# Optimization experiments

Hardware: AMD Instinct MI355X
Metric: run time of the kernel (lower is better)

The kernel has to match this reference:

```python
import jax, jax.numpy as jnp
import numpy as np

B, N, C = 2, 2048, 768
H = 16
D = C // H  # head_dim = 48
SCALE = 1.0 / float(np.sqrt(D))


def setup_inputs() -> dict:
    key = jax.random.key(0)
    ks = jax.random.split(key, 5)
    x = jax.random.normal(ks[0], (B, N, C), dtype=jnp.float32)
    # torch nn.Linear weights are [out, in]; apply as x @ W.T
    qkv_w = jax.random.normal(ks[1], (3 * C, C), dtype=jnp.float32) * 0.02
    qkv_b = jax.random.normal(ks[2], (3 * C,), dtype=jnp.float32) * 0.02
    proj_w = jax.random.normal(ks[3], (C, C), dtype=jnp.float32) * 0.02
    proj_b = jax.random.normal(ks[4], (C,), dtype=jnp.float32) * 0.02
    return {"x": x, "qkv_w": qkv_w, "qkv_b": qkv_b, "proj_w": proj_w, "proj_b": proj_b}


def reference(x, qkv_w, qkv_b, proj_w, proj_b):
    # qkv: (B, N, 3C) -> (3, B, H, N, D)
    qkv = x @ qkv_w.T + qkv_b
    qkv = qkv.reshape(B, N, 3, H, D).transpose(2, 0, 3, 1, 4)
    q, k, v = qkv[0], qkv[1], qkv[2]
    # manual attention: full (B, H, N, N) score matrix, as in the original
    attn = jnp.einsum('bhqd,bhkd->bhqk', q, k) * SCALE
    attn = jax.nn.softmax(attn, axis=-1)
    # attn_drop with p=0.0 (eval / deterministic) is identity
    y = jnp.einsum('bhqk,bhkd->bhqd', attn, v)
    y = y.transpose(0, 2, 1, 3).reshape(B, N, C)
    return y @ proj_w.T + proj_b
```

## Files before the change

### kernel.cpp

```cpp
#include <hip/hip_runtime.h>

typedef short v8s __attribute__((ext_vector_type(8)));
typedef short v4s __attribute__((ext_vector_type(4)));
typedef float v4f __attribute__((ext_vector_type(4)));
typedef unsigned uint2v __attribute__((ext_vector_type(2)));
typedef unsigned uint4v __attribute__((ext_vector_type(4)));
typedef unsigned short u16;

#define NSEQ 2048
#define CDIM 768
#define NH   16
#define DH   48
#define DP   64
#define MROWS 4096
#define N3C  2304
#define BH   32

#if __has_builtin(__builtin_amdgcn_exp2f)
#define EXP2(x) __builtin_amdgcn_exp2f(x)
#else
#define EXP2(x) exp2f(x)
#endif
#if __has_builtin(__builtin_amdgcn_rcpf)
#define RCP(x) __builtin_amdgcn_rcpf(x)
#else
#define RCP(x) (1.0f/(x))
#endif

#if __has_builtin(__builtin_amdgcn_permlane32_swap) && __has_builtin(__builtin_amdgcn_permlane16_swap)
#define HAVE_PERMSWAP 1
#endif

__device__ __forceinline__ u16 f2bf(float f){
  unsigned u = __float_as_uint(f);
  u += 0x7FFFu + ((u>>16)&1u);
  return (u16)(u>>16);
}

#if __has_builtin(__builtin_amdgcn_cvt_pk_bf16_f32)
typedef __bf16 bf16x2_t __attribute__((ext_vector_type(2)));
__device__ __forceinline__ unsigned pkbf(float a, float b){
  bf16x2_t r = __builtin_amdgcn_cvt_pk_bf16_f32(a, b);
  return __builtin_bit_cast(unsigned, r);
}
#else
__device__ __forceinline__ unsigned pkbf(float a, float b){
  unsigned x = __float_as_uint(a), y = __float_as_uint(b);
  x += 0x7FFFu + ((x>>16)&1u);
  y += 0x7FFFu + ((y>>16)&1u);
  return (x>>16) | (y & 0xFFFF0000u);
}
#endif

__device__ __forceinline__ void load_lds16(const u16* g, u16* l){
  __builtin_amdgcn_global_load_lds((const __attribute__((address_space(1))) void*)g,
                                   (__attribute__((address_space(3))) void*)l, 16, 0, 0);
}

#define XN8  (MROWS*CDIM/8)
#define WN8  (N3C*CDIM/8)
#define PN8  (CDIM*CDIM/8)
#define CONVB ((XN8+WN8+PN8)/256)
__global__ __launch_bounds__(256) void prep(const float* __restrict__ x, const float* __restrict__ w,
                                            const float* __restrict__ pw, u16* __restrict__ dst,
                                            u16* __restrict__ q, u16* __restrict__ k){
  int bid = blockIdx.x;
  if (bid < CONVB){
    int i = bid*256 + threadIdx.x;
    const float* src;
    if (i < XN8)            src = x  + (size_t)i*8;
    else if (i < XN8+WN8)   src = w  + (size_t)(i - XN8)*8;
    else                    src = pw + (size_t)(i - XN8 - WN8)*8;
    v4f f0 = ((const v4f*)src)[0];
    v4f f1 = ((const v4f*)src)[1];
    v8s o;
#pragma unroll
    for (int j = 0; j < 4; j++) ((u16*)&o)[j]   = f2bf(f0[j]);
#pragma unroll
    for (int j = 0; j < 4; j++) ((u16*)&o)[4+j] = f2bf(f1[j]);
    ((v8s*)dst)[i] = o;
  } else {
    int idx = (bid - CONVB)*256 + threadIdx.x;
    v8s z = (v8s){0,0,0,0,0,0,0,0};
    int r = idx >> 1, half = idx & 1;
    *(v8s*)(q + (size_t)r*DP + DH + half*8) = z;
    *(v8s*)(k + (size_t)r*DP + DH + half*8) = z;
  }
}

__global__ __launch_bounds__(256) void qkv_gemm(const u16* __restrict__ x, const u16* __restrict__ w,
                                                const float* __restrict__ bias,
                                                u16* __restrict__ q, u16* __restrict__ k, u16* __restrict__ v){
  __shared__ __align__(16) u16 As[128*32];
  __shared__ __align__(16) u16 Bs[128*32];
  const int wave = threadIdx.x >> 6;
  const int lane = threadIdx.x & 63;
  const int l15  = lane & 15;
  const int quad = lane >> 4;
  const int wm = wave & 1, wn = wave >> 1;
  const int m0 = blockIdx.x*128, n0 = blockIdx.y*128;

  const int srow = lane >> 2;
  const int sg   = (lane & 3) ^ ((lane >> 3) & 3);
  const int sgoff = sg*8;

  v4f acc[4][4];
#pragma unroll
  for (int i = 0; i < 4; i++)
#pragma unroll
    for (int j = 0; j < 4; j++) acc[i][j] = (v4f){0.f,0.f,0.f,0.f};

  const int sig = (l15 >> 1) & 3;

  for (int kt = 0; kt < CDIM/32; kt++){
    const int k0 = kt*32;
    __syncthreads();
#pragma unroll
    for (int j = 0; j < 2; j++){
      int c = wave*2 + j;
      int r = c*16 + srow;
      load_lds16(x + (size_t)(m0 + r)*CDIM + k0 + sgoff, &As[c*512]);
      load_lds16(w + (size_t)(n0 + r)*CDIM + k0 + sgoff, &Bs[c*512]);
    }
    __syncthreads();

    v8s af[4], bf[4];
#pragma unroll
    for (int t = 0; t < 4; t++){
      int ra = wm*64 + t*16 + l15;
      af[t] = *(const v8s*)(&As[ra*32 + ((quad ^ sig)<<3)]);
      int rb = wn*64 + t*16 + l15;
      bf[t] = *(const v8s*)(&Bs[rb*32 + ((quad ^ sig)<<3)]);
    }
#pragma unroll
    for (int ti = 0; ti < 4; ti++)
#pragma unroll
      for (int tj = 0; tj < 4; tj++)
        acc[ti][tj] = __builtin_amdgcn_mfma_f32_16x16x32_bf16(af[ti], bf[tj], acc[ti][tj], 0, 0, 0);
  }

  const float QS = 0.2082540589f;
#pragma unroll
  for (int tj = 0; tj < 4; tj++){
    const int c = n0 + wn*64 + tj*16 + l15;
    const float bv = bias[c];
    const int t = c / CDIM;
    const int rem = c - t*CDIM;
    const int h = rem / DH;
    const int d = rem - h*DH;
#pragma unroll
    for (int ti = 0; ti < 4; ti++){
#pragma unroll
      for (int r = 0; r < 4; r++){
        int m = m0 + wm*64 + ti*16 + quad*4 + r;
        int b_ = m >> 11;
        int n  = m & (NSEQ-1);
        float val = acc[ti][tj][r] + bv;
        if (t == 0) val *= QS;
        u16 o  = f2bf(val);
        int bhn = b_*NH + h;
        if (t == 0)      q[((size_t)bhn*NSEQ + n)*DP + d] = o;
        else if (t == 1) k[((size_t)bhn*NSEQ + n)*DP + d] = o;
        else             v[((size_t)bhn*DP + d)*NSEQ + n] = o;
      }
    }
  }
}

__global__ __launch_bounds__(256, 4) void attn(const u16* __restrict__ q, const u16* __restrict__ k,
                                               const u16* __restrict__ v,
                                               float* __restrict__ oacc, float* __restrict__ lacc){
  __shared__ __align__(16) u16 Kl[2][64*64];
  __shared__ __align__(16) u16 Vl[2][48*64];
#ifndef HAVE_PERMSWAP
  __shared__ __align__(16) u16 Pl[4*2*1024];
#endif
  const int bh = blockIdx.x;
  const int qt = blockIdx.y;
  const int sp = blockIdx.z;
  const int wave = threadIdx.x >> 6;
  const int lane = threadIdx.x & 63;
  const int l15  = lane & 15;
  const int quad = lane >> 4;
  const int lo3  = l15 & 7;
  const u16* qb = q + (size_t)bh*NSEQ*DP;
  const u16* kb = k + (size_t)bh*NSEQ*DP;
  const u16* vb = v + (size_t)bh*DP*NSEQ;
  const int qm = qt*128 + wave*32;

  v8s qf[2][2];
#pragma unroll
  for (int si = 0; si < 2; si++)
#pragma unroll
    for (int ks = 0; ks < 2; ks++)
      qf[si][ks] = *(const v8s*)(qb + (size_t)(qm + si*16 + l15)*DP + ks*32 + quad*8);

  const short one = (short)0x3F80;
  const v8s vones = (l15 == 0) ? (v8s){one,one,one,one,one,one,one,one}
                               : (v8s){0,0,0,0,0,0,0,0};

  v4f o[2][4];
#pragma unroll
  for (int si = 0; si < 2; si++)
#pragma unroll
    for (int i = 0; i < 4; i++) o[si][i] = (v4f){0.f,0.f,0.f,0.f};

  const int sr  = lane >> 3;
  const int soff = ((lane & 7) ^ (sr & 7)) * 8;
#ifndef HAVE_PERMSWAP
  u16* Plw = Pl + wave*2048;
#endif

  const int krow0 = wave*8 + sr;
#define STAGE(kt_, b_) do{                                                              \
    load_lds16(kb + ((size_t)((kt_)*64 + krow0))*DP + soff,      &Kl[b_][krow0*64]);    \
    load_lds16(kb + ((size_t)((kt_)*64 + 32 + krow0))*DP + soff, &Kl[b_][(32+krow0)*64]);\
    load_lds16(vb + (size_t)krow0*NSEQ + (kt_)*64 + soff,        &Vl[b_][krow0*64]);    \
    if (wave < 2)                                                                       \
      load_lds16(vb + (size_t)(32+krow0)*NSEQ + (kt_)*64 + soff, &Vl[b_][(32+krow0)*64]);\
  } while(0)

  STAGE(sp*16, 0);

  for (int i = 0; i < 16; i++){
    const int buf = i & 1;
    __syncthreads();
    if (i < 15) STAGE(sp*16 + i + 1, buf^1);

    const u16* Klb = &Kl[buf][0];
    const u16* Vlb = &Vl[buf][0];

    v4f s[2][4];
#pragma unroll
    for (int nt = 0; nt < 4; nt++){
      int rrow = nt*16 + l15;
      v8s kf0 = *(const v8s*)(&Klb[rrow*64 + ((quad ^ lo3)<<3)]);
      v8s kf1 = *(const v8s*)(&Klb[rrow*64 + (((4+quad) ^ lo3)<<3)]);
      s[0][nt] = __builtin_amdgcn_mfma_f32_16x16x32_bf16(kf0, qf[0][0], (v4f){0.f,0.f,0.f,0.f}, 0, 0, 0);
      s[0][nt] = __builtin_amdgcn_mfma_f32_16x16x32_bf16(kf1, qf[0][1], s[0][nt], 0, 0, 0);
      s[1][nt] = __builtin_amdgcn_mfma_f32_16x16x32_bf16(kf0, qf[1][0], (v4f){0.f,0.f,0.f,0.f}, 0, 0, 0);
      s[1][nt] = __builtin_amdgcn_mfma_f32_16x16x32_bf16(kf1, qf[1][1], s[1][nt], 0, 0, 0);
    }

    v8s pa[2][2];
#ifdef HAVE_PERMSWAP
#pragma unroll
    for (int si = 0; si < 2; si++){
      unsigned w[4][2];
#pragma unroll
      for (int nt = 0; nt < 4; nt++){
        w[nt][0] = pkbf(EXP2(s[si][nt][0]), EXP2(s[si][nt][1]));
        w[nt][1] = pkbf(EXP2(s[si][nt][2]), EXP2(s[si][nt][3]));
      }
#pragma unroll
      for (int ks = 0; ks < 2; ks++){
        unsigned W[4];
#pragma unroll
        for (int h = 0; h < 2; h++){
          auto a = __builtin_amdgcn_permlane32_swap(w[2*ks][h], w[2*ks+1][h], false, false);
          auto b = __builtin_amdgcn_permlane16_swap(a[0], a[1], false, false);
          W[h]   = b[0];
          W[2+h] = b[1];
        }
        uint4v u; u[0] = W[0]; u[1] = W[1]; u[2] = W[2]; u[3] = W[3];
        pa[si][ks] = __builtin_bit_cast(v8s, u);
      }
    }
#else
#pragma unroll
    for (int si = 0; si < 2; si++)
#pragma unroll
      for (int nt = 0; nt < 4; nt++){
        uint2v pw;
        pw.x = pkbf(EXP2(s[si][nt][0]), EXP2(s[si][nt][1]));
        pw.y = pkbf(EXP2(s[si][nt][2]), EXP2(s[si][nt][3]));
        int g = nt*2 + (quad>>1);
        *(uint2v*)(&Plw[si*1024 + l15*64 + ((g ^ lo3)<<3) + (quad&1)*4]) = pw;
      }
#pragma unroll
    for (int si = 0; si < 2; si++)
#pragma unroll
      for (int ks = 0; ks < 2; ks++){
        int ga = ks*4 + quad;
        pa[si][ks] = *(const v8s*)(&Plw[si*1024 + l15*64 + ((ga ^ lo3)<<3)]);
      }
#endif

#pragma unroll
    for (int dt = 0; dt < 3; dt++){
#pragma unroll
      for (int ks = 0; ks < 2; ks++){
        int row = dt*16 + l15;
        v8s vf = *(const v8s*)(&Vlb[row*64 + (((ks*4+quad) ^ lo3)<<3)]);
        o[0][dt] = __builtin_amdgcn_mfma_f32_16x16x32_bf16(pa[0][ks], vf, o[0][dt], 0, 0, 0);
        o[1][dt] = __builtin_amdgcn_mfma_f32_16x16x32_bf16(pa[1][ks], vf, o[1][dt], 0, 0, 0);
      }
    }
#pragma unroll
    for (int ks = 0; ks < 2; ks++){
      o[0][3] = __builtin_amdgcn_mfma_f32_16x16x32_bf16(pa[0][ks], vones, o[0][3], 0, 0, 0);
      o[1][3] = __builtin_amdgcn_mfma_f32_16x16x32_bf16(pa[1][ks], vones, o[1][3], 0, 0, 0);
    }
  }

  const int b_ = bh / NH, h = bh % NH;
  float* oa = oacc + (size_t)sp*MROWS*CDIM;
  float* la = lacc + (size_t)sp*MROWS*NH;
#pragma unroll
  for (int si = 0; si < 2; si++){
#pragma unroll
    for (int r = 0; r < 4; r++){
      int rowg = b_*NSEQ + qm + si*16 + quad*4 + r;
#pragma unroll
      for (int dt = 0; dt < 3; dt++)
        oa[(size_t)rowg*CDIM + h*DH + dt*16 + l15] = o[si][dt][r];
      if (l15 == 0) la[rowg*NH + h] = o[si][3][r];
    }
  }
}

__global__ __launch_bounds__(256) void finalize(const float* __restrict__ oacc,
                                                const float* __restrict__ lacc,
                                                u16* __restrict__ y){
  int i = blockIdx.x*256 + threadIdx.x;
  int rowg = i / 192, c4 = i - rowg*192;
  int c = c4*4, h = c / DH;
  float l = lacc[rowg*NH + h] + lacc[MROWS*NH + rowg*NH + h];
  float inv = RCP(l);
  v4f a = *(const v4f*)(oacc + (size_t)rowg*CDIM + c);
  v4f b = *(const v4f*)(oacc + (size_t)MROWS*CDIM + (size_t)rowg*CDIM + c);
  v4s o4;
#pragma unroll
  for (int j = 0; j < 4; j++) o4[j] = (short)f2bf((a[j] + b[j])*inv);
  *(v4s*)(y + (size_t)rowg*CDIM + c) = o4;
}

__global__ __launch_bounds__(256) void proj_gemm(const u16* __restrict__ y, const u16* __restrict__ w,
                                                 const float* __restrict__ bias, float* __restrict__ out){
  __shared__ __align__(16) u16 As[64*32];
  __shared__ __align__(16) u16 Bs[128*32];
  const int wave = threadIdx.x >> 6;
  const int lane = threadIdx.x & 63;
  const int l15  = lane & 15;
  const int quad = lane >> 4;
  const int wm = wave & 1, wn = wave >> 1;
  const int m0 = blockIdx.x*64, n0 = blockIdx.y*128;

  const int srow = lane >> 2;
  const int sg   = (lane & 3) ^ ((lane >> 3) & 3);
  const int sgoff = sg*8;

  v4f acc[2][4];
#pragma unroll
  for (int i = 0; i < 2; i++)
#pragma unroll
    for (int j = 0; j < 4; j++) acc[i][j] = (v4f){0.f,0.f,0.f,0.f};

  const int sig = (l15 >> 1) & 3;

  for (int kt = 0; kt < CDIM/32; kt++){
    const int k0 = kt*32;
    __syncthreads();
    {
      int rA = wave*16 + srow;
      load_lds16(y + (size_t)(m0 + rA)*CDIM + k0 + sgoff, &As[wave*512]);
#pragma unroll
      for (int j = 0; j < 2; j++){
        int c = wave*2 + j;
        int rB = c*16 + srow;
        load_lds16(w + (size_t)(n0 + rB)*CDIM + k0 + sgoff, &Bs[c*512]);
      }
    }
    __syncthreads();

    v8s af[2], bf[4];
#pragma unroll
    for (int t = 0; t < 2; t++){
      int ra = wm*32 + t*16 + l15;
      af[t] = *(const v8s*)(&As[ra*32 + ((quad ^ sig)<<3)]);
    }
#pragma unroll
    for (int t = 0; t < 4; t++){
      int rb = wn*64 + t*16 + l15;
      bf[t] = *(const v8s*)(&Bs[rb*32 + ((quad ^ sig)<<3)]);
    }
#pragma unroll
    for (int ti = 0; ti < 2; ti++)
#pragma unroll
      for (int tj = 0; tj < 4; tj++)
        acc[ti][tj] = __builtin_amdgcn_mfma_f32_16x16x32_bf16(af[ti], bf[tj], acc[ti][tj], 0, 0, 0);
  }

#pragma unroll
  for (int tj = 0; tj < 4; tj++){
    const int c = n0 + wn*64 + tj*16 + l15;
    const float bv = bias[c];
#pragma unroll
    for (int ti = 0; ti < 2; ti++){
#pragma unroll
      for (int r = 0; r < 4; r++){
        int m = m0 + wm*32 + ti*16 + quad*4 + r;
        out[(size_t)m*CDIM + c] = acc[ti][tj][r] + bv;
      }
    }
  }
}

extern "C" void kernel_launch(void* const* d_in, const int* in_sizes, int n_in,
                              void* d_out, int out_size, void* d_ws, size_t ws_size,
                              hipStream_t stream){
  const float* x      = (const float*)d_in[0];
  const float* qkv_w  = (const float*)d_in[1];
  const float* qkv_b  = (const float*)d_in[2];
  const float* proj_w = (const float*)d_in[3];
  const float* proj_b = (const float*)d_in[4];
  float* out = (float*)d_out;

  u16* xb  = (u16*)d_ws;
  u16* wb  = xb  + (size_t)MROWS*CDIM;
  u16* pwb = wb  + (size_t)N3C*CDIM;
  u16* q   = pwb + (size_t)CDIM*CDIM;
  u16* k   = q + (size_t)BH*NSEQ*DP;
  u16* v   = k + (size_t)BH*NSEQ*DP;
  float* oacc = (float*)(v + (size_t)BH*NSEQ*DP);
  float* lacc = oacc + (size_t)2*MROWS*CDIM;
  u16* y = xb;

  prep<<<dim3(CONVB + 512), dim3(256), 0, stream>>>(x, qkv_w, proj_w, xb, q, k);
  qkv_gemm<<<dim3(MROWS/128, N3C/128), dim3(256), 0, stream>>>(xb, wb, qkv_b, q, k, v);
  attn<<<dim3(BH, NSEQ/128, 2), dim3(256), 0, stream>>>(q, k, v, oacc, lacc);
  finalize<<<dim3(MROWS*192/256), dim3(256), 0, stream>>>(oacc, lacc, y);
  proj_gemm<<<dim3(MROWS/64, CDIM/128), dim3(256), 0, stream>>>(y, pwb, proj_b, out);
}
```

Baseline: 168.1 us.

## Double-buffer LDS in QKV and projection GEMMs, shrink projection tile

Both GEMM kernels now use two LDS buffers. The next k-tile's global-to-LDS load is issued right after a single barrier, so it overlaps with the MFMA work on the current tile, and one of the two barriers per iteration is removed. The projection GEMM tile also shrinks from 64x128 to 64x64, which doubles the number of blocks for better occupancy across CUs. This relies on the barrier waiting for the outstanding async LDS loads. The change uses more LDS in the QKV GEMM and does less work per block in the projection GEMM.

```diff
diff --git a/kernel.cpp b/kernel.cpp
--- a/kernel.cpp
+++ b/kernel.cpp
@@ -91,8 +91,8 @@
 __global__ __launch_bounds__(256) void qkv_gemm(const u16* __restrict__ x, const u16* __restrict__ w,
                                                 const float* __restrict__ bias,
                                                 u16* __restrict__ q, u16* __restrict__ k, u16* __restrict__ v){
-  __shared__ __align__(16) u16 As[128*32];
-  __shared__ __align__(16) u16 Bs[128*32];
+  __shared__ __align__(16) u16 As[2][128*32];
+  __shared__ __align__(16) u16 Bs[2][128*32];
   const int wave = threadIdx.x >> 6;
   const int lane = threadIdx.x & 63;
   const int l15  = lane & 15;
@@ -112,25 +112,30 @@
 
   const int sig = (l15 >> 1) & 3;
 
+#define QSTAGE(kt_, b_) do{                                                         \
+    _Pragma("unroll")                                                               \
+    for (int j = 0; j < 2; j++){                                                    \
+      int c = wave*2 + j;                                                           \
+      int r = c*16 + srow;                                                          \
+      load_lds16(x + (size_t)(m0 + r)*CDIM + (kt_)*32 + sgoff, &As[b_][c*512]);     \
+      load_lds16(w + (size_t)(n0 + r)*CDIM + (kt_)*32 + sgoff, &Bs[b_][c*512]);     \
+    }                                                                               \
+  } while(0)
+
+  QSTAGE(0, 0);
+
   for (int kt = 0; kt < CDIM/32; kt++){
-    const int k0 = kt*32;
+    const int buf = kt & 1;
     __syncthreads();
-#pragma unroll
-    for (int j = 0; j < 2; j++){
-      int c = wave*2 + j;
-      int r = c*16 + srow;
-      load_lds16(x + (size_t)(m0 + r)*CDIM + k0 + sgoff, &As[c*512]);
-      load_lds16(w + (size_t)(n0 + r)*CDIM + k0 + sgoff, &Bs[c*512]);
-    }
-    __syncthreads();
+    if (kt < CDIM/32 - 1) QSTAGE(kt+1, buf^1);
 
     v8s af[4], bf[4];
 #pragma unroll
     for (int t = 0; t < 4; t++){
       int ra = wm*64 + t*16 + l15;
-      af[t] = *(const v8s*)(&As[ra*32 + ((quad ^ sig)<<3)]);
+      af[t] = *(const v8s*)(&As[buf][ra*32 + ((quad ^ sig)<<3)]);
       int rb = wn*64 + t*16 + l15;
-      bf[t] = *(const v8s*)(&Bs[rb*32 + ((quad ^ sig)<<3)]);
+      bf[t] = *(const v8s*)(&Bs[buf][rb*32 + ((quad ^ sig)<<3)]);
     }
 #pragma unroll
     for (int ti = 0; ti < 4; ti++)
@@ -138,6 +143,7 @@
       for (int tj = 0; tj < 4; tj++)
         acc[ti][tj] = __builtin_amdgcn_mfma_f32_16x16x32_bf16(af[ti], bf[tj], acc[ti][tj], 0, 0, 0);
   }
+#undef QSTAGE
 
   const float QS = 0.2082540589f;
 #pragma unroll
@@ -337,63 +343,59 @@
 
 __global__ __launch_bounds__(256) void proj_gemm(const u16* __restrict__ y, const u16* __restrict__ w,
                                                  const float* __restrict__ bias, float* __restrict__ out){
-  __shared__ __align__(16) u16 As[64*32];
-  __shared__ __align__(16) u16 Bs[128*32];
+  __shared__ __align__(16) u16 As[2][64*32];
+  __shared__ __align__(16) u16 Bs[2][64*32];
   const int wave = threadIdx.x >> 6;
   const int lane = threadIdx.x & 63;
   const int l15  = lane & 15;
   const int quad = lane >> 4;
   const int wm = wave & 1, wn = wave >> 1;
-  const int m0 = blockIdx.x*64, n0 = blockIdx.y*128;
+  const int m0 = blockIdx.x*64, n0 = blockIdx.y*64;
 
   const int srow = lane >> 2;
   const int sg   = (lane & 3) ^ ((lane >> 3) & 3);
   const int sgoff = sg*8;
 
-  v4f acc[2][4];
+  v4f acc[2][2];
 #pragma unroll
   for (int i = 0; i < 2; i++)
 #pragma unroll
-    for (int j = 0; j < 4; j++) acc[i][j] = (v4f){0.f,0.f,0.f,0.f};
+    for (int j = 0; j < 2; j++) acc[i][j] = (v4f){0.f,0.f,0.f,0.f};
 
   const int sig = (l15 >> 1) & 3;
+  const int rS = wave*16 + srow;
+
+#define PSTAGE(kt_, b_) do{                                                          \
+    load_lds16(y + (size_t)(m0 + rS)*CDIM + (kt_)*32 + sgoff, &As[b_][wave*512]);    \
+    load_lds16(w + (size_t)(n0 + rS)*CDIM + (kt_)*32 + sgoff, &Bs[b_][wave*512]);    \
+  } while(0)
+
+  PSTAGE(0, 0);
 
   for (int kt = 0; kt < CDIM/32; kt++){
-    const int k0 = kt*32;
+    const int buf = kt & 1;
     __syncthreads();
-    {
-      int rA = wave*16 + srow;
-      load_lds16(y + (size_t)(m0 + rA)*CDIM + k0 + sgoff, &As[wave*512]);
-#pragma unroll
-      for (int j = 0; j < 2; j++){
-        int c = wave*2 + j;
-        int rB = c*16 + srow;
-        load_lds16(w + (size_t)(n0 + rB)*CDIM + k0 + sgoff, &Bs[c*512]);
-      }
-    }
-    __syncthreads();
-
-    v8s af[2], bf[4];
+    if (kt < CDIM/32 - 1) PSTAGE(kt+1, buf^1);
+
+    v8s af[2], bf[2];
 #pragma unroll
     for (int t = 0; t < 2; t++){
       int ra = wm*32 + t*16 + l15;
-      af[t] = *(const v8s*)(&As[ra*32 + ((quad ^ sig)<<3)]);
-    }
-#pragma unroll
-    for (int t = 0; t < 4; t++){
-      int rb = wn*64 + t*16 + l15;
-      bf[t] = *(const v8s*)(&Bs[rb*32 + ((quad ^ sig)<<3)]);
+      af[t] = *(const v8s*)(&As[buf][ra*32 + ((quad ^ sig)<<3)]);
+      int rb = wn*32 + t*16 + l15;
+      bf[t] = *(const v8s*)(&Bs[buf][rb*32 + ((quad ^ sig)<<3)]);
     }
 #pragma unroll
     for (int ti = 0; ti < 2; ti++)
 #pragma unroll
-      for (int tj = 0; tj < 4; tj++)
+      for (int tj = 0; tj < 2; tj++)
         acc[ti][tj] = __builtin_amdgcn_mfma_f32_16x16x32_bf16(af[ti], bf[tj], acc[ti][tj], 0, 0, 0);
   }
-
-#pragma unroll
-  for (int tj = 0; tj < 4; tj++){
-    const int c = n0 + wn*64 + tj*16 + l15;
+#undef PSTAGE
+
+#pragma unroll
+  for (int tj = 0; tj < 2; tj++){
+    const int c = n0 + wn*32 + tj*16 + l15;
     const float bv = bias[c];
 #pragma unroll
     for (int ti = 0; ti < 2; ti++){
@@ -430,5 +432,5 @@
   qkv_gemm<<<dim3(MROWS/128, N3C/128), dim3(256), 0, stream>>>(xb, wb, qkv_b, q, k, v);
   attn<<<dim3(BH, NSEQ/128, 2), dim3(256), 0, stream>>>(q, k, v, oacc, lacc);
   finalize<<<dim3(MROWS*192/256), dim3(256), 0, stream>>>(oacc, lacc, y);
-  proj_gemm<<<dim3(MROWS/64, CDIM/128), dim3(256), 0, stream>>>(y, pwb, proj_b, out);
-}
+  proj_gemm<<<dim3(MROWS/64, CDIM/64), dim3(256), 0, stream>>>(y, pwb, proj_b, out);
+}
```

Result: slower. 177.7 us (+5.7%).

## Store Q transposed with permlane-packed vector epilogue stores and add MFMA setprio

Applied to the files above, without the earlier changes.

Q now uses a d-major layout like V, so the QKV GEMM epilogue for Q and V can pack bf16 pairs, shuffle them with permlane swaps and write 16-byte vector stores instead of scattered 2-byte stores. The attention kernel gathers Q fragments with strided scalar loads, issued after the first K/V stage so they overlap it. The zero-padding kernel is adjusted to the new Q layout. s_setprio is raised around the MFMA blocks to favour matrix issue across waves. The strided Q gather is an extra cost paid once per attention block.

```diff
diff --git a/kernel.cpp b/kernel.cpp
--- a/kernel.cpp
+++ b/kernel.cpp
@@ -83,8 +83,10 @@
     int idx = (bid - CONVB)*256 + threadIdx.x;
     v8s z = (v8s){0,0,0,0,0,0,0,0};
     int r = idx >> 1, half = idx & 1;
-    *(v8s*)(q + (size_t)r*DP + DH + half*8) = z;
     *(v8s*)(k + (size_t)r*DP + DH + half*8) = z;
+    int bhn = idx >> 12, rem = idx & 4095;
+    int dd = rem >> 8, nc = rem & 255;
+    *(v8s*)(q + ((size_t)bhn*DP + DH + dd)*NSEQ + nc*8) = z;
   }
 }
 
@@ -140,28 +142,66 @@
   }
 
   const float QS = 0.2082540589f;
-#pragma unroll
-  for (int tj = 0; tj < 4; tj++){
-    const int c = n0 + wn*64 + tj*16 + l15;
-    const float bv = bias[c];
-    const int t = c / CDIM;
-    const int rem = c - t*CDIM;
-    const int h = rem / DH;
-    const int d = rem - h*DH;
-#pragma unroll
-    for (int ti = 0; ti < 4; ti++){
-#pragma unroll
-      for (int r = 0; r < 4; r++){
-        int m = m0 + wm*64 + ti*16 + quad*4 + r;
-        int b_ = m >> 11;
-        int n  = m & (NSEQ-1);
-        float val = acc[ti][tj][r] + bv;
-        if (t == 0) val *= QS;
-        u16 o  = f2bf(val);
-        int bhn = b_*NH + h;
-        if (t == 0)      q[((size_t)bhn*NSEQ + n)*DP + d] = o;
-        else if (t == 1) k[((size_t)bhn*NSEQ + n)*DP + d] = o;
-        else             v[((size_t)bhn*DP + d)*NSEQ + n] = o;
+  const int t    = blockIdx.y / 6;
+  const int nseg = (blockIdx.y - t*6)*128;
+  const int b_   = m0 >> 11;
+
+#ifdef HAVE_PERMSWAP
+  if (t != 1){
+    u16* dst = (t == 0) ? q : v;
+#pragma unroll
+    for (int tj = 0; tj < 4; tj++){
+      const int cs = nseg + wn*64 + tj*16 + l15;
+      const float bv = bias[t*CDIM + cs];
+      const int h = cs / DH;
+      const int d = cs - h*DH;
+      u16* rowp = dst + ((size_t)(b_*NH + h)*DP + d)*NSEQ;
+      unsigned wd[4][2];
+#pragma unroll
+      for (int ti = 0; ti < 4; ti++){
+        float v0 = acc[ti][tj][0] + bv, v1 = acc[ti][tj][1] + bv;
+        float v2 = acc[ti][tj][2] + bv, v3 = acc[ti][tj][3] + bv;
+        if (t == 0){ v0 *= QS; v1 *= QS; v2 *= QS; v3 *= QS; }
+        wd[ti][0] = pkbf(v0, v1);
+        wd[ti][1] = pkbf(v2, v3);
+      }
+#pragma unroll
+      for (int ks = 0; ks < 2; ks++){
+        unsigned W[4];
+#pragma unroll
+        for (int hh = 0; hh < 2; hh++){
+          auto a = __builtin_amdgcn_permlane32_swap(wd[2*ks][hh], wd[2*ks+1][hh], false, false);
+          auto b = __builtin_amdgcn_permlane16_swap(a[0], a[1], false, false);
+          W[hh]   = b[0];
+          W[2+hh] = b[1];
+        }
+        uint4v u; u[0] = W[0]; u[1] = W[1]; u[2] = W[2]; u[3] = W[3];
+        const int n = (m0 & (NSEQ-1)) + wm*64 + ks*32 + quad*8;
+        *(uint4v*)(rowp + n) = u;
+      }
+    }
+  } else
+#endif
+  {
+#pragma unroll
+    for (int tj = 0; tj < 4; tj++){
+      const int cs = nseg + wn*64 + tj*16 + l15;
+      const float bv = bias[t*CDIM + cs];
+      const int h = cs / DH;
+      const int d = cs - h*DH;
+      const int bhn = b_*NH + h;
+#pragma unroll
+      for (int ti = 0; ti < 4; ti++){
+#pragma unroll
+        for (int r = 0; r < 4; r++){
+          int n = (m0 & (NSEQ-1)) + wm*64 + ti*16 + quad*4 + r;
+          float val = acc[ti][tj][r] + bv;
+          if (t == 0) val *= QS;
+          u16 o = f2bf(val);
+          if (t == 0)      q[((size_t)bhn*DP + d)*NSEQ + n] = o;
+          else if (t == 1) k[((size_t)bhn*NSEQ + n)*DP + d] = o;
+          else             v[((size_t)bhn*DP + d)*NSEQ + n] = o;
+        }
       }
     }
   }
@@ -183,27 +223,10 @@
   const int l15  = lane & 15;
   const int quad = lane >> 4;
   const int lo3  = l15 & 7;
-  const u16* qb = q + (size_t)bh*NSEQ*DP;
+  const u16* qb = q + (size_t)bh*DP*NSEQ;
   const u16* kb = k + (size_t)bh*NSEQ*DP;
   const u16* vb = v + (size_t)bh*DP*NSEQ;
   const int qm = qt*128 + wave*32;
-
-  v8s qf[2][2];
-#pragma unroll
-  for (int si = 0; si < 2; si++)
-#pragma unroll
-    for (int ks = 0; ks < 2; ks++)
-      qf[si][ks] = *(const v8s*)(qb + (size_t)(qm + si*16 + l15)*DP + ks*32 + quad*8);
-
-  const short one = (short)0x3F80;
-  const v8s vones = (l15 == 0) ? (v8s){one,one,one,one,one,one,one,one}
-                               : (v8s){0,0,0,0,0,0,0,0};
-
-  v4f o[2][4];
-#pragma unroll
-  for (int si = 0; si < 2; si++)
-#pragma unroll
-    for (int i = 0; i < 4; i++) o[si][i] = (v4f){0.f,0.f,0.f,0.f};
 
   const int sr  = lane >> 3;
   const int soff = ((lane & 7) ^ (sr & 7)) * 8;
@@ -222,6 +245,28 @@
 
   STAGE(sp*16, 0);
 
+  v8s qf[2][2];
+#pragma unroll
+  for (int si = 0; si < 2; si++)
+#pragma unroll
+    for (int ks = 0; ks < 2; ks++){
+      v8s tq;
+#pragma unroll
+      for (int j = 0; j < 8; j++)
+        ((u16*)&tq)[j] = qb[(size_t)(ks*32 + quad*8 + j)*NSEQ + qm + si*16 + l15];
+      qf[si][ks] = tq;
+    }
+
+  const short one = (short)0x3F80;
+  const v8s vones = (l15 == 0) ? (v8s){one,one,one,one,one,one,one,one}
+                               : (v8s){0,0,0,0,0,0,0,0};
+
+  v4f o[2][4];
+#pragma unroll
+  for (int si = 0; si < 2; si++)
+#pragma unroll
+    for (int i = 0; i < 4; i++) o[si][i] = (v4f){0.f,0.f,0.f,0.f};
+
   for (int i = 0; i < 16; i++){
     const int buf = i & 1;
     __syncthreads();
@@ -231,6 +276,7 @@
     const u16* Vlb = &Vl[buf][0];
 
     v4f s[2][4];
+    __builtin_amdgcn_s_setprio(1);
 #pragma unroll
     for (int nt = 0; nt < 4; nt++){
       int rrow = nt*16 + l15;
@@ -241,6 +287,7 @@
       s[1][nt] = __builtin_amdgcn_mfma_f32_16x16x32_bf16(kf0, qf[1][0], (v4f){0.f,0.f,0.f,0.f}, 0, 0, 0);
       s[1][nt] = __builtin_amdgcn_mfma_f32_16x16x32_bf16(kf1, qf[1][1], s[1][nt], 0, 0, 0);
     }
+    __builtin_amdgcn_s_setprio(0);
 
     v8s pa[2][2];
 #ifdef HAVE_PERMSWAP
@@ -286,6 +333,7 @@
       }
 #endif
 
+    __builtin_amdgcn_s_setprio(1);
 #pragma unroll
     for (int dt = 0; dt < 3; dt++){
 #pragma unroll
@@ -301,6 +349,7 @@
       o[0][3] = __builtin_amdgcn_mfma_f32_16x16x32_bf16(pa[0][ks], vones, o[0][3], 0, 0, 0);
       o[1][3] = __builtin_amdgcn_mfma_f32_16x16x32_bf16(pa[1][ks], vones, o[1][3], 0, 0, 0);
     }
+    __builtin_amdgcn_s_setprio(0);
   }
 
   const int b_ = bh / NH, h = bh % NH;
```

Measured after the change: 175.8 us. 4.6% more time.

## Drop split-KV in attention and normalize output in-kernel, removing finalize

Applied to the files above, without the earlier changes.

The attention kernel no longer splits the key sequence into two halves across a grid z-dimension. Each block now walks all 32 key tiles and normalizes its output with the row sum obtained by a lane shuffle. It then writes bf16 y directly, which removes the fp32 partial buffers and the separate finalize kernel along with their global traffic and launch. The cost is half as many attention blocks (512 rather than 1024), each running a loop twice as long, so the GPU has less parallelism to fill its compute units.

```diff
diff --git a/kernel.cpp b/kernel.cpp
--- a/kernel.cpp
+++ b/kernel.cpp
@@ -168,8 +168,7 @@
 }
 
 __global__ __launch_bounds__(256, 4) void attn(const u16* __restrict__ q, const u16* __restrict__ k,
-                                               const u16* __restrict__ v,
-                                               float* __restrict__ oacc, float* __restrict__ lacc){
+                                               const u16* __restrict__ v, u16* __restrict__ y){
   __shared__ __align__(16) u16 Kl[2][64*64];
   __shared__ __align__(16) u16 Vl[2][48*64];
 #ifndef HAVE_PERMSWAP
@@ -177,7 +176,6 @@
 #endif
   const int bh = blockIdx.x;
   const int qt = blockIdx.y;
-  const int sp = blockIdx.z;
   const int wave = threadIdx.x >> 6;
   const int lane = threadIdx.x & 63;
   const int l15  = lane & 15;
@@ -220,12 +218,12 @@
       load_lds16(vb + (size_t)(32+krow0)*NSEQ + (kt_)*64 + soff, &Vl[b_][(32+krow0)*64]);\
   } while(0)
 
-  STAGE(sp*16, 0);
-
-  for (int i = 0; i < 16; i++){
+  STAGE(0, 0);
+
+  for (int i = 0; i < 32; i++){
     const int buf = i & 1;
     __syncthreads();
-    if (i < 15) STAGE(sp*16 + i + 1, buf^1);
+    if (i < 31) STAGE(i + 1, buf^1);
 
     const u16* Klb = &Kl[buf][0];
     const u16* Vlb = &Vl[buf][0];
@@ -304,35 +302,18 @@
   }
 
   const int b_ = bh / NH, h = bh % NH;
-  float* oa = oacc + (size_t)sp*MROWS*CDIM;
-  float* la = lacc + (size_t)sp*MROWS*NH;
 #pragma unroll
   for (int si = 0; si < 2; si++){
 #pragma unroll
     for (int r = 0; r < 4; r++){
+      float l = __shfl(o[si][3][r], (lane & 48));
+      float inv = RCP(l);
       int rowg = b_*NSEQ + qm + si*16 + quad*4 + r;
 #pragma unroll
       for (int dt = 0; dt < 3; dt++)
-        oa[(size_t)rowg*CDIM + h*DH + dt*16 + l15] = o[si][dt][r];
-      if (l15 == 0) la[rowg*NH + h] = o[si][3][r];
-    }
-  }
-}
-
-__global__ __launch_bounds__(256) void finalize(const float* __restrict__ oacc,
-                                                const float* __restrict__ lacc,
-                                                u16* __restrict__ y){
-  int i = blockIdx.x*256 + threadIdx.x;
-  int rowg = i / 192, c4 = i - rowg*192;
-  int c = c4*4, h = c / DH;
-  float l = lacc[rowg*NH + h] + lacc[MROWS*NH + rowg*NH + h];
-  float inv = RCP(l);
-  v4f a = *(const v4f*)(oacc + (size_t)rowg*CDIM + c);
-  v4f b = *(const v4f*)(oacc + (size_t)MROWS*CDIM + (size_t)rowg*CDIM + c);
-  v4s o4;
-#pragma unroll
-  for (int j = 0; j < 4; j++) o4[j] = (short)f2bf((a[j] + b[j])*inv);
-  *(v4s*)(y + (size_t)rowg*CDIM + c) = o4;
+        y[(size_t)rowg*CDIM + h*DH + dt*16 + l15] = f2bf(o[si][dt][r]*inv);
+    }
+  }
 }
 
 __global__ __launch_bounds__(256) void proj_gemm(const u16* __restrict__ y, const u16* __restrict__ w,
@@ -422,13 +403,10 @@
   u16* q   = pwb + (size_t)CDIM*CDIM;
   u16* k   = q + (size_t)BH*NSEQ*DP;
   u16* v   = k + (size_t)BH*NSEQ*DP;
-  float* oacc = (float*)(v + (size_t)BH*NSEQ*DP);
-  float* lacc = oacc + (size_t)2*MROWS*CDIM;
   u16* y = xb;
 
   prep<<<dim3(CONVB + 512), dim3(256), 0, stream>>>(x, qkv_w, proj_w, xb, q, k);
   qkv_gemm<<<dim3(MROWS/128, N3C/128), dim3(256), 0, stream>>>(xb, wb, qkv_b, q, k, v);
-  attn<<<dim3(BH, NSEQ/128, 2), dim3(256), 0, stream>>>(q, k, v, oacc, lacc);
-  finalize<<<dim3(MROWS*192/256), dim3(256), 0, stream>>>(oacc, lacc, y);
+  attn<<<dim3(BH, NSEQ/128), dim3(256), 0, stream>>>(q, k, v, y);
   proj_gemm<<<dim3(MROWS/64, CDIM/128), dim3(256), 0, stream>>>(y, pwb, proj_b, out);
 }
```

Measured after the change: 165.6 us. About the same (-1.5%).
